# Kernel tuning notes

Measured on AMD Instinct MI355X. Metric: run time of the kernel, lower is better.

Reference implementation:

```python
import jax, jax.numpy as jnp
import numpy as np

N_NODES = 100_000
N_EDGES = 3_200_000
EPS_BN = 1e-5
EPS_NORM = 1e-12


def _sage_conv(x, src, dst, ew, pw, pb, lw, lb, rw, n_nodes):
    # project=True: relu(Linear_in->in) applied to source features
    xp = jax.nn.relu(x @ pw + pb)                       # [N, in]
    msg = xp[src] * ew[:, None]                         # [E, in] gather + weight
    agg = jax.ops.segment_sum(msg, dst, num_segments=n_nodes)      # scatter-sum
    cnt = jax.ops.segment_sum(jnp.ones_like(ew), dst, num_segments=n_nodes)
    mean = agg / jnp.maximum(cnt, 1.0)[:, None]         # scatter-mean
    out = mean @ lw + lb + x @ rw                       # neighbor lin + root lin
    # normalize=True: L2 normalize rows
    nrm = jnp.sqrt(jnp.sum(out * out, axis=-1, keepdims=True))
    return out / jnp.maximum(nrm, EPS_NORM)


def setup_inputs() -> dict:
    key = jax.random.key(0)
    ks = jax.random.split(key, 20)
    d = {}
    d["h"] = jax.random.normal(ks[0], (N_NODES, 5), dtype=jnp.float32)
    d["edge_index"] = jax.random.randint(ks[1], (2, N_EDGES), 0, N_NODES, dtype=jnp.int32)
    d["edge_weight"] = jax.random.uniform(ks[2], (N_EDGES,), dtype=jnp.float32)
    # BatchNorm1d(5) params (conv2_norm in the source is unused in forward)
    d["bn_gamma"] = jnp.ones((5,), jnp.float32)
    d["bn_beta"] = jnp.zeros((5,), jnp.float32)

    def lin(k, fan_in, fan_out):
        return jax.random.normal(k, (fan_in, fan_out), jnp.float32) * (1.0 / np.sqrt(fan_in))

    # conv1: 5 -> 64 ; conv2: 64 -> 64 (fixing source bug) ; conv3: 64 -> 5
    dims = [(5, 64), (64, 64), (64, 5)]
    ki = 3
    for i, (fi, fo) in enumerate(dims, start=1):
        d[f"c{i}_pw"] = lin(ks[ki], fi, fi); ki += 1
        d[f"c{i}_pb"] = jnp.zeros((fi,), jnp.float32)
        d[f"c{i}_lw"] = lin(ks[ki], fi, fo); ki += 1
        d[f"c{i}_lb"] = jnp.zeros((fo,), jnp.float32)
        d[f"c{i}_rw"] = lin(ks[ki], fi, fo); ki += 1
    return d


def reference(h, edge_index, edge_weight, bn_gamma, bn_beta,
              c1_pw, c1_pb, c1_lw, c1_lb, c1_rw,
              c2_pw, c2_pb, c2_lw, c2_lb, c2_rw,
              c3_pw, c3_pb, c3_lw, c3_lb, c3_rw):
    src, dst = edge_index[0], edge_index[1]
    # BatchNorm1d (training-mode batch statistics, biased variance)
    mu = jnp.mean(h, axis=0)
    var = jnp.mean((h - mu) ** 2, axis=0)
    x = (h - mu) * jax.lax.rsqrt(var + EPS_BN) * bn_gamma + bn_beta

    x = jax.nn.relu(_sage_conv(x, src, dst, edge_weight, c1_pw, c1_pb, c1_lw, c1_lb, c1_rw, N_NODES))
    x = jax.nn.relu(_sage_conv(x, src, dst, edge_weight, c2_pw, c2_pb, c2_lw, c2_lb, c2_rw, N_NODES))
    x = _sage_conv(x, src, dst, edge_weight, c3_pw, c3_pb, c3_lw, c3_lb, c3_rw, N_NODES)
    # dropout omitted (deterministic / eval-mode reference)
    return x
```

## Files before the change

kernel.cpp:

```cpp
#include <hip/hip_runtime.h>
#include <hip/hip_bf16.h>

#define N_NODES 100000
#define N_EDGES 3200000
#define BSH 8
#define NB 391

typedef __hip_bfloat16 bf16;

#define RL(v, k) __int_as_float(__builtin_amdgcn_readlane(__float_as_int(v), (k)))

__device__ __forceinline__ float loadF(const void* p, long long i, int isf32) {
    if (isf32) return ((const float*)p)[i];
    unsigned short v = ((const unsigned short*)p)[i];
    union { unsigned u; float f; } c;
    c.u = ((unsigned)v) << 16;
    return c.f;
}

__device__ __forceinline__ unsigned packEdge(int s, float w) {
    bf16 b = __float2bfloat16(w);
    unsigned short bits = *(unsigned short*)&b;
    return ((unsigned)s << 15) | (unsigned)(bits & 0x7FFF);
}
__device__ __forceinline__ int edgeSrc(unsigned u) { return (int)(u >> 15); }
__device__ __forceinline__ float edgeW(unsigned u) {
    union { unsigned x; float f; } c;
    c.x = (u & 0x7FFFu) << 16;
    return c.f;
}

#define W_GAMMA 0
#define W_BETA 8
#define W_C1PW 16
#define W_C1PB 48
#define W_C1LW 56
#define W_C1LB 376
#define W_C1RW 440
#define W_C2PW 760
#define W_C2PB 4856
#define W_C2LW 4920
#define W_C2LB 9016
#define W_C2RW 9080
#define W_C3PW 13176
#define W_C3PB 17272
#define W_C3LW 17336
#define W_C3LB 17656
#define W_C3RW 17664

__global__ void detect_dtype(const void* ew, int* flag) {
    const unsigned short* u = (const unsigned short*)ew;
    int lane = threadIdx.x;
    int big = 0;
    for (int i = lane; i < 1024; i += 64) {
        unsigned short v = u[2 * i];
        int ex = (v >> 7) & 0xFF;
        if (ex >= 128) big++;
    }
#pragma unroll
    for (int o = 32; o; o >>= 1) big += __shfl_xor(big, o, 64);
    if (lane == 0) *flag = (big > 100) ? 1 : 0;
}

__global__ void cvt_weights(const int* flag,
                            const void* p0, const void* p1, const void* p2, const void* p3,
                            const void* p4, const void* p5, const void* p6, const void* p7,
                            const void* p8, const void* p9, const void* p10, const void* p11,
                            const void* p12, const void* p13, const void* p14, const void* p15,
                            const void* p16, float* __restrict__ wts) {
    const void* ptrs[17] = {p0, p1, p2, p3, p4, p5, p6, p7, p8,
                            p9, p10, p11, p12, p13, p14, p15, p16};
    const int sz[17] = {5, 5, 25, 5, 320, 64, 320, 4096, 64,
                        4096, 64, 4096, 4096, 64, 320, 5, 320};
    const int off[17] = {W_GAMMA, W_BETA, W_C1PW, W_C1PB, W_C1LW, W_C1LB, W_C1RW,
                         W_C2PW, W_C2PB, W_C2LW, W_C2LB, W_C2RW,
                         W_C3PW, W_C3PB, W_C3LW, W_C3LB, W_C3RW};
    int t = blockIdx.x;
    int isf32 = *flag;
    for (int i = threadIdx.x; i < sz[t]; i += blockDim.x)
        wts[off[t] + i] = loadF(ptrs[t], i, isf32);
}

__global__ void bn_stats(const void* __restrict__ h, const int* __restrict__ flag,
                         float* __restrict__ stats) {
    int isf32 = *flag;
    float s[5] = {0, 0, 0, 0, 0}, q[5] = {0, 0, 0, 0, 0};
    int tid = blockIdx.x * blockDim.x + threadIdx.x;
    int stride = gridDim.x * blockDim.x;
    for (int i = tid; i < N_NODES; i += stride) {
#pragma unroll
        for (int f = 0; f < 5; f++) {
            float v = loadF(h, i * 5 + f, isf32);
            s[f] += v;
            q[f] += v * v;
        }
    }
#pragma unroll
    for (int f = 0; f < 5; f++) {
#pragma unroll
        for (int o = 32; o; o >>= 1) {
            s[f] += __shfl_xor(s[f], o, 64);
            q[f] += __shfl_xor(q[f], o, 64);
        }
    }
    __shared__ float ls[4][10];
    int wave = threadIdx.x >> 6, lane = threadIdx.x & 63;
    if (lane == 0) {
#pragma unroll
        for (int f = 0; f < 5; f++) { ls[wave][f] = s[f]; ls[wave][5 + f] = q[f]; }
    }
    __syncthreads();
    if (threadIdx.x < 10) {
        float v = ls[0][threadIdx.x] + ls[1][threadIdx.x] + ls[2][threadIdx.x] + ls[3][threadIdx.x];
        int idx = (threadIdx.x < 5) ? threadIdx.x : (threadIdx.x - 5 + 8);
        atomicAdd(&stats[idx], v);
    }
}

__global__ void bn_proj1(const void* __restrict__ h, const int* __restrict__ flag,
                         const float* __restrict__ stats, const float* __restrict__ wts,
                         float* __restrict__ xbn, float* __restrict__ xp1) {
    __shared__ float s_sc[5], s_sb[5];
    if (threadIdx.x < 5) {
        int f = threadIdx.x;
        float mean = stats[f] / (float)N_NODES;
        float var = stats[8 + f] / (float)N_NODES - mean * mean;
        float sc = wts[W_GAMMA + f] * rsqrtf(var + 1e-5f);
        s_sc[f] = sc;
        s_sb[f] = wts[W_BETA + f] - mean * sc;
    }
    __syncthreads();
    int isf32 = *flag;
    int i = blockIdx.x * blockDim.x + threadIdx.x;
    if (i >= N_NODES) return;
    float x[5];
#pragma unroll
    for (int f = 0; f < 5; f++)
        x[f] = loadF(h, i * 5 + f, isf32) * s_sc[f] + s_sb[f];
#pragma unroll
    for (int f = 0; f < 5; f++) xbn[i * 5 + f] = x[f];
#pragma unroll
    for (int j = 0; j < 5; j++) {
        float a = wts[W_C1PB + j];
#pragma unroll
        for (int k = 0; k < 5; k++) a += x[k] * wts[W_C1PW + k * 5 + j];
        xp1[i * 5 + j] = fmaxf(a, 0.f);
    }
}

__global__ void __launch_bounds__(256) bucket_hist(const int* __restrict__ dst,
                                                   int* __restrict__ bucketCnt) {
    __shared__ int hcnt[NB];
    for (int i = threadIdx.x; i < NB; i += 256) hcnt[i] = 0;
    __syncthreads();
    int per = (N_EDGES + gridDim.x - 1) / gridDim.x;
    int s = blockIdx.x * per;
    int e = min(s + per, N_EDGES);
    for (int i = s + threadIdx.x; i < e; i += 256)
        atomicAdd(&hcnt[dst[i] >> BSH], 1);
    __syncthreads();
    for (int i = threadIdx.x; i < NB; i += 256)
        if (hcnt[i]) atomicAdd(&bucketCnt[i], hcnt[i]);
}

__global__ void __launch_bounds__(512) bucket_scan(const int* __restrict__ bucketCnt,
                                                   int* __restrict__ bucketStart,
                                                   int* __restrict__ bucketCursor) {
    int tid = threadIdx.x, lane = tid & 63, w = tid >> 6;
    int v = (tid < NB) ? bucketCnt[tid] : 0;
    int sc = v;
#pragma unroll
    for (int o = 1; o < 64; o <<= 1) {
        int t = __shfl_up(sc, o, 64);
        if (lane >= o) sc += t;
    }
    __shared__ int ws[8];
    if (lane == 63) ws[w] = sc;
    __syncthreads();
    if (w == 0) {
        int wv = (lane < 8) ? ws[lane] : 0;
        int s2 = wv;
#pragma unroll
        for (int o = 1; o < 8; o <<= 1) {
            int t = __shfl_up(s2, o, 64);
            if (lane >= o) s2 += t;
        }
        if (lane < 8) ws[lane] = s2;
    }
    __syncthreads();
    int woff = w ? ws[w - 1] : 0;
    int ex = woff + sc - v;
    if (tid < NB) {
        bucketStart[tid] = ex;
        bucketCursor[tid] = ex;
    }
    if (tid == 0) bucketStart[NB] = N_EDGES;
}

__global__ void __launch_bounds__(256) bucket_stage(const int* __restrict__ src,
                                                    const int* __restrict__ dst,
                                                    const void* __restrict__ ew,
                                                    const int* __restrict__ flag,
                                                    int* __restrict__ bucketCursor,
                                                    uint2* __restrict__ stage) {
    __shared__ int hcnt[NB], cur[NB];
    int isf32 = *flag;
    for (int i = threadIdx.x; i < NB; i += 256) hcnt[i] = 0;
    __syncthreads();
    int per = (N_EDGES + gridDim.x - 1) / gridDim.x;
    int s = blockIdx.x * per;
    int e = min(s + per, N_EDGES);
    for (int i = s + threadIdx.x; i < e; i += 256)
        atomicAdd(&hcnt[dst[i] >> BSH], 1);
    __syncthreads();
    for (int i = threadIdx.x; i < NB; i += 256)
        cur[i] = hcnt[i] ? atomicAdd(&bucketCursor[i], hcnt[i]) : 0;
    __syncthreads();
    for (int i = s + threadIdx.x; i < e; i += 256) {
        int d = dst[i];
        int slot = atomicAdd(&cur[d >> BSH], 1);
        stage[slot] = make_uint2((unsigned)d, packEdge(src[i], loadF(ew, i, isf32)));
    }
}

__global__ void __launch_bounds__(256) bucket_place(const uint2* __restrict__ stage,
                                                    const int* __restrict__ bucketStart,
                                                    int* __restrict__ start,
                                                    unsigned* __restrict__ perm) {
    int b = blockIdx.x, tid = threadIdx.x;
    int base = bucketStart[b];
    int cnt = bucketStart[b + 1] - base;
    int n0 = b << BSH;
    int nn = min(256, N_NODES - n0);
    __shared__ int lcnt[256], loff[256], ws[4];
    lcnt[tid] = 0;
    __syncthreads();
    for (int i = tid; i < cnt; i += 256)
        atomicAdd(&lcnt[stage[base + i].x & 255], 1);
    __syncthreads();
    int lane = tid & 63, w = tid >> 6;
    int v = lcnt[tid];
    int sc = v;
#pragma unroll
    for (int o = 1; o < 64; o <<= 1) {
        int t = __shfl_up(sc, o, 64);
        if (lane >= o) sc += t;
    }
    if (lane == 63) ws[w] = sc;
    __syncthreads();
    int woff = 0;
    for (int k = 0; k < w; k++) woff += ws[k];
    loff[tid] = woff + sc - v;
    __syncthreads();
    if (tid < nn) start[n0 + tid] = base + loff[tid];
    if (b == 0 && tid == 0) start[N_NODES] = N_EDGES;
    lcnt[tid] = 0;
    __syncthreads();
    for (int i = tid; i < cnt; i += 256) {
        uint2 sv = stage[base + i];
        int l = sv.x & 255;
        int p = atomicAdd(&lcnt[l], 1);
        perm[base + loff[l] + p] = sv.y;
    }
}

__global__ void __launch_bounds__(256) conv1_fused(const float* __restrict__ xp1,
                                                   const float* __restrict__ xbn,
                                                   const int* __restrict__ start,
                                                   const unsigned* __restrict__ perm,
                                                   const float* __restrict__ wts,
                                                   float* __restrict__ x1,
                                                   bf16* __restrict__ y2) {
    int lane = threadIdx.x & 63;
    int wid = __builtin_amdgcn_readfirstlane((blockIdx.x * blockDim.x + threadIdx.x) >> 6);
    int nw = (gridDim.x * blockDim.x) >> 6;
    float Wlw[5], Wrw[5];
#pragma unroll
    for (int k = 0; k < 5; k++) {
        Wlw[k] = wts[W_C1LW + k * 64 + lane];
        Wrw[k] = wts[W_C1RW + k * 64 + lane];
    }
    float lb = wts[W_C1LB + lane];
    float W1[64], W2[64];
#pragma unroll
    for (int k = 0; k < 64; k++) W1[k] = wts[W_C2PW + k * 64 + lane];
#pragma unroll
    for (int k = 0; k < 64; k++) W2[k] = wts[W_C2LW + k * 64 + lane];
    float pb = wts[W_C2PB + lane];
    for (int node = wid; node < N_NODES; node += nw) {
        int e0 = start[node], e1 = start[node + 1];
        float s0 = 0, s1 = 0, s2 = 0, s3 = 0, s4 = 0;
        for (int eb = e0; eb < e1; eb += 64) {
            int e = eb + lane;
            if (e < e1) {
                unsigned p = perm[e];
                float w = edgeW(p);
                const float* row = xp1 + (size_t)edgeSrc(p) * 5;
                s0 += row[0] * w; s1 += row[1] * w; s2 += row[2] * w;
                s3 += row[3] * w; s4 += row[4] * w;
            }
        }
#pragma unroll
        for (int o = 32; o; o >>= 1) {
            s0 += __shfl_xor(s0, o, 64);
            s1 += __shfl_xor(s1, o, 64);
            s2 += __shfl_xor(s2, o, 64);
            s3 += __shfl_xor(s3, o, 64);
            s4 += __shfl_xor(s4, o, 64);
        }
        float ic = 1.f / fmaxf((float)(e1 - e0), 1.f);
        float xb = (lane < 5) ? xbn[node * 5 + lane] : 0.f;
        float out = lb + s0 * ic * Wlw[0] + s1 * ic * Wlw[1] + s2 * ic * Wlw[2] +
                    s3 * ic * Wlw[3] + s4 * ic * Wlw[4];
#pragma unroll
        for (int k = 0; k < 5; k++) out += RL(xb, k) * Wrw[k];
        float ss = out * out;
#pragma unroll
        for (int o = 32; o; o >>= 1) ss += __shfl_xor(ss, o, 64);
        float xv = fmaxf(out / fmaxf(sqrtf(ss), 1e-12f), 0.f);
        x1[(size_t)node * 64 + lane] = xv;
        float a0 = pb, a1 = 0.f, a2 = 0.f, a3 = 0.f;
#pragma unroll
        for (int k = 0; k < 64; k += 4) {
            a0 += RL(xv, k) * W1[k];
            a1 += RL(xv, k + 1) * W1[k + 1];
            a2 += RL(xv, k + 2) * W1[k + 2];
            a3 += RL(xv, k + 3) * W1[k + 3];
        }
        float xp = fmaxf((a0 + a1) + (a2 + a3), 0.f);
        float b0 = 0.f, b1 = 0.f, b2 = 0.f, b3 = 0.f;
#pragma unroll
        for (int k = 0; k < 64; k += 4) {
            b0 += RL(xp, k) * W2[k];
            b1 += RL(xp, k + 1) * W2[k + 1];
            b2 += RL(xp, k + 2) * W2[k + 2];
            b3 += RL(xp, k + 3) * W2[k + 3];
        }
        y2[(size_t)node * 64 + lane] = __float2bfloat16((b0 + b1) + (b2 + b3));
    }
}

__global__ void __launch_bounds__(256) conv2_fused_reg(const bf16* __restrict__ y2,
                                                       const int* __restrict__ start,
                                                       const unsigned* __restrict__ perm,
                                                       const float* __restrict__ x1,
                                                       const float* __restrict__ wts,
                                                       float* __restrict__ x2) {
    int lane = threadIdx.x & 63;
    int wid = __builtin_amdgcn_readfirstlane((blockIdx.x * blockDim.x + threadIdx.x) >> 6);
    int nw = (gridDim.x * blockDim.x) >> 6;
    float W[64];
#pragma unroll
    for (int k = 0; k < 64; k++) W[k] = wts[W_C2RW + k * 64 + lane];
    float lb = wts[W_C2LB + lane];
    for (int node = wid; node < N_NODES; node += nw) {
        int e0 = start[node], e1 = start[node + 1];
        float acc = 0.f;
        int e = e0;
        for (; e + 16 <= e1; e += 16) {
            unsigned p[16];
#pragma unroll
            for (int u = 0; u < 16; u++) p[u] = perm[e + u];
            float v[16];
#pragma unroll
            for (int u = 0; u < 16; u++)
                v[u] = __bfloat162float(y2[(size_t)edgeSrc(p[u]) * 64 + lane]);
#pragma unroll
            for (int u = 0; u < 16; u++) acc += v[u] * edgeW(p[u]);
        }
        for (; e + 4 <= e1; e += 4) {
            unsigned p[4];
#pragma unroll
            for (int u = 0; u < 4; u++) p[u] = perm[e + u];
            float v[4];
#pragma unroll
            for (int u = 0; u < 4; u++)
                v[u] = __bfloat162float(y2[(size_t)edgeSrc(p[u]) * 64 + lane]);
#pragma unroll
            for (int u = 0; u < 4; u++) acc += v[u] * edgeW(p[u]);
        }
        for (; e < e1; e++) {
            unsigned p = perm[e];
            acc += __bfloat162float(y2[(size_t)edgeSrc(p) * 64 + lane]) * edgeW(p);
        }
        float ic = 1.f / fmaxf((float)(e1 - e0), 1.f);
        float xv = x1[(size_t)node * 64 + lane];
        float o0 = acc * ic + lb, o1 = 0.f, o2 = 0.f, o3 = 0.f;
#pragma unroll
        for (int k = 0; k < 64; k += 4) {
            o0 += RL(xv, k) * W[k];
            o1 += RL(xv, k + 1) * W[k + 1];
            o2 += RL(xv, k + 2) * W[k + 2];
            o3 += RL(xv, k + 3) * W[k + 3];
        }
        float out = (o0 + o1) + (o2 + o3);
        float ss = out * out;
#pragma unroll
        for (int o = 32; o; o >>= 1) ss += __shfl_xor(ss, o, 64);
        float v = out / fmaxf(sqrtf(ss), 1e-12f);
        x2[(size_t)node * 64 + lane] = fmaxf(v, 0.f);
    }
}

__global__ void __launch_bounds__(256) proj3_reg(const float* __restrict__ x2,
                                                 const float* __restrict__ wts,
                                                 float* __restrict__ y3) {
    int lane = threadIdx.x & 63;
    int wid = __builtin_amdgcn_readfirstlane((blockIdx.x * blockDim.x + threadIdx.x) >> 6);
    int nw = (gridDim.x * blockDim.x) >> 6;
    float W1[64], Wl[5];
#pragma unroll
    for (int k = 0; k < 64; k++) W1[k] = wts[W_C3PW + k * 64 + lane];
#pragma unroll
    for (int j = 0; j < 5; j++) Wl[j] = wts[W_C3LW + lane * 5 + j];
    float pb = wts[W_C3PB + lane];
    for (int node = wid; node < N_NODES; node += nw) {
        float xv = x2[(size_t)node * 64 + lane];
        float a0 = pb, a1 = 0.f, a2 = 0.f, a3 = 0.f;
#pragma unroll
        for (int k = 0; k < 64; k += 4) {
            a0 += RL(xv, k) * W1[k];
            a1 += RL(xv, k + 1) * W1[k + 1];
            a2 += RL(xv, k + 2) * W1[k + 2];
            a3 += RL(xv, k + 3) * W1[k + 3];
        }
        float xp = fmaxf((a0 + a1) + (a2 + a3), 0.f);
#pragma unroll
        for (int j = 0; j < 5; j++) {
            float p = xp * Wl[j];
#pragma unroll
            for (int o = 32; o; o >>= 1) p += __shfl_xor(p, o, 64);
            if (lane == j) y3[node * 5 + j] = p;
        }
    }
}

__global__ void __launch_bounds__(256) conv3_fused(const float* __restrict__ y3,
                                                   const float* __restrict__ x2,
                                                   const int* __restrict__ start,
                                                   const unsigned* __restrict__ perm,
                                                   const float* __restrict__ wts,
                                                   const int* __restrict__ flag,
                                                   void* __restrict__ outp) {
    int lane = threadIdx.x & 63;
    int wid = __builtin_amdgcn_readfirstlane((blockIdx.x * blockDim.x + threadIdx.x) >> 6);
    int nw = (gridDim.x * blockDim.x) >> 6;
    float Wr[5];
#pragma unroll
    for (int j = 0; j < 5; j++) Wr[j] = wts[W_C3RW + lane * 5 + j];
    float lb3[5];
#pragma unroll
    for (int j = 0; j < 5; j++) lb3[j] = wts[W_C3LB + j];
    int isf32 = *flag;
    for (int node = wid; node < N_NODES; node += nw) {
        int e0 = start[node], e1 = start[node + 1];
        float s0 = 0, s1 = 0, s2 = 0, s3 = 0, s4 = 0;
        for (int eb = e0; eb < e1; eb += 64) {
            int e = eb + lane;
            if (e < e1) {
                unsigned p = perm[e];
                float w = edgeW(p);
                const float* row = y3 + (size_t)edgeSrc(p) * 5;
                s0 += row[0] * w; s1 += row[1] * w; s2 += row[2] * w;
                s3 += row[3] * w; s4 += row[4] * w;
            }
        }
#pragma unroll
        for (int o = 32; o; o >>= 1) {
            s0 += __shfl_xor(s0, o, 64);
            s1 += __shfl_xor(s1, o, 64);
            s2 += __shfl_xor(s2, o, 64);
            s3 += __shfl_xor(s3, o, 64);
            s4 += __shfl_xor(s4, o, 64);
        }
        float ic = 1.f / fmaxf((float)(e1 - e0), 1.f);
        float xv = x2[(size_t)node * 64 + lane];
        float m[5] = {s0 * ic, s1 * ic, s2 * ic, s3 * ic, s4 * ic};
        float r[5], ss = 0.f;
#pragma unroll
        for (int j = 0; j < 5; j++) {
            float p = xv * Wr[j];
#pragma unroll
            for (int o = 32; o; o >>= 1) p += __shfl_xor(p, o, 64);
            r[j] = p + m[j] + lb3[j];
            ss += r[j] * r[j];
        }
        float inv = 1.f / fmaxf(sqrtf(ss), 1e-12f);
#pragma unroll
        for (int j = 0; j < 5; j++) {
            if (lane == j) {
                float v = r[j] * inv;
                if (isf32) ((float*)outp)[node * 5 + j] = v;
                else ((bf16*)outp)[node * 5 + j] = __float2bfloat16(v);
            }
        }
    }
}

extern "C" void kernel_launch(void* const* d_in, const int* in_sizes, int n_in,
                              void* d_out, int out_size, void* d_ws, size_t ws_size,
                              hipStream_t stream) {
    const void* h = d_in[0];
    const int* ei = (const int*)d_in[1];
    const int* src = ei;
    const int* dst = ei + N_EDGES;
    const void* ew = d_in[2];

    float* W = (float*)d_ws;
    int* flag = (int*)W;
    float* stats = W + 16;
    float* wts = W + 64;
    float* xbn = W + 20480;
    float* xp1 = xbn + N_NODES * 5;
    int* startp = (int*)(xp1 + N_NODES * 5);
    int* bucketCnt = startp + N_NODES + 64;
    int* bucketStart = bucketCnt + NB + 1;
    int* bucketCursor = bucketStart + NB + 1;
    unsigned* perm = (unsigned*)(bucketCursor + NB + 62);
    float* x1 = (float*)(perm + N_EDGES);
    uint2* stage = (uint2*)x1;
    bf16* y2 = (bf16*)(x1 + (size_t)N_NODES * 64);
    float* x2 = x1;
    float* y3 = xp1;

    detect_dtype<<<1, 64, 0, stream>>>(ew, flag);
    cvt_weights<<<17, 256, 0, stream>>>(flag,
        d_in[3], d_in[4],
        d_in[5], d_in[6], d_in[7], d_in[8], d_in[9],
        d_in[10], d_in[11], d_in[12], d_in[13], d_in[14],
        d_in[15], d_in[16], d_in[17], d_in[18], d_in[19],
        wts);

    hipMemsetAsync(stats, 0, 32 * sizeof(float), stream);
    hipMemsetAsync(bucketCnt, 0, NB * sizeof(int), stream);

    bn_stats<<<200, 256, 0, stream>>>(h, flag, stats);
    bn_proj1<<<(N_NODES + 255) / 256, 256, 0, stream>>>(h, flag, stats, wts, xbn, xp1);

    bucket_hist<<<256, 256, 0, stream>>>(dst, bucketCnt);
    bucket_scan<<<1, 512, 0, stream>>>(bucketCnt, bucketStart, bucketCursor);
    bucket_stage<<<256, 256, 0, stream>>>(src, dst, ew, flag, bucketCursor, stage);
    bucket_place<<<NB, 256, 0, stream>>>(stage, bucketStart, startp, perm);

    conv1_fused<<<2048, 256, 0, stream>>>(xp1, xbn, startp, perm, wts, x1, y2);

    conv2_fused_reg<<<4096, 256, 0, stream>>>(y2, startp, perm, x1, wts, x2);

    proj3_reg<<<1024, 256, 0, stream>>>(x2, wts, y3);
    conv3_fused<<<2048, 256, 0, stream>>>(y3, x2, startp, perm, wts, flag, d_out);
}
```

Measured before the change: 574.1 us.

## Fuse layer-3 projection into conv2 and pad 5-wide node rows to 8 floats

The layer-3 projection (relu(x2·W3p + b) followed by the 5-wide neighbor linear) is folded into the conv2 kernel's epilogue, so x2 no longer has to be re-read by a separate kernel and one launch is dropped. The 5-float per-node rows for xp1 and y3 are padded to a stride of 8 so that the conv1 and conv3 edge gathers can use one aligned float4 load plus one scalar load. The bucket histogram and staging kernels also get twice as many blocks. The cost is 69 more weight registers held per lane in conv2, which may lower occupancy for its latency-bound gather, and the padded rows take more workspace memory.

```diff
diff --git a/kernel.cpp b/kernel.cpp
--- a/kernel.cpp
+++ b/kernel.cpp
@@ -144,7 +144,7 @@
         float a = wts[W_C1PB + j];
 #pragma unroll
         for (int k = 0; k < 5; k++) a += x[k] * wts[W_C1PW + k * 5 + j];
-        xp1[i * 5 + j] = fmaxf(a, 0.f);
+        xp1[i * 8 + j] = fmaxf(a, 0.f);
     }
 }
 
@@ -295,9 +295,11 @@
             if (e < e1) {
                 unsigned p = perm[e];
                 float w = edgeW(p);
-                const float* row = xp1 + (size_t)edgeSrc(p) * 5;
-                s0 += row[0] * w; s1 += row[1] * w; s2 += row[2] * w;
-                s3 += row[3] * w; s4 += row[4] * w;
+                const float* row = xp1 + (size_t)edgeSrc(p) * 8;
+                float4 v4 = *(const float4*)row;
+                float v5 = row[4];
+                s0 += v4.x * w; s1 += v4.y * w; s2 += v4.z * w;
+                s3 += v4.w * w; s4 += v5 * w;
             }
         }
 #pragma unroll
@@ -340,12 +342,13 @@
     }
 }
 
-__global__ void __launch_bounds__(256) conv2_fused_reg(const bf16* __restrict__ y2,
-                                                       const int* __restrict__ start,
-                                                       const unsigned* __restrict__ perm,
-                                                       const float* __restrict__ x1,
-                                                       const float* __restrict__ wts,
-                                                       float* __restrict__ x2) {
+__global__ void __launch_bounds__(256) conv2_fused3(const bf16* __restrict__ y2,
+                                                    const int* __restrict__ start,
+                                                    const unsigned* __restrict__ perm,
+                                                    const float* __restrict__ x1,
+                                                    const float* __restrict__ wts,
+                                                    float* __restrict__ x2,
+                                                    float* __restrict__ y3) {
     int lane = threadIdx.x & 63;
     int wid = __builtin_amdgcn_readfirstlane((blockIdx.x * blockDim.x + threadIdx.x) >> 6);
     int nw = (gridDim.x * blockDim.x) >> 6;
@@ -353,6 +356,12 @@
 #pragma unroll
     for (int k = 0; k < 64; k++) W[k] = wts[W_C2RW + k * 64 + lane];
     float lb = wts[W_C2LB + lane];
+    float W3[64], Wl3[5];
+#pragma unroll
+    for (int k = 0; k < 64; k++) W3[k] = wts[W_C3PW + k * 64 + lane];
+#pragma unroll
+    for (int j = 0; j < 5; j++) Wl3[j] = wts[W_C3LW + lane * 5 + j];
+    float pb3 = wts[W_C3PB + lane];
     for (int node = wid; node < N_NODES; node += nw) {
         int e0 = start[node], e1 = start[node + 1];
         float acc = 0.f;
@@ -397,40 +406,23 @@
         float ss = out * out;
 #pragma unroll
         for (int o = 32; o; o >>= 1) ss += __shfl_xor(ss, o, 64);
-        float v = out / fmaxf(sqrtf(ss), 1e-12f);
-        x2[(size_t)node * 64 + lane] = fmaxf(v, 0.f);
-    }
-}
-
-__global__ void __launch_bounds__(256) proj3_reg(const float* __restrict__ x2,
-                                                 const float* __restrict__ wts,
-                                                 float* __restrict__ y3) {
-    int lane = threadIdx.x & 63;
-    int wid = __builtin_amdgcn_readfirstlane((blockIdx.x * blockDim.x + threadIdx.x) >> 6);
-    int nw = (gridDim.x * blockDim.x) >> 6;
-    float W1[64], Wl[5];
-#pragma unroll
-    for (int k = 0; k < 64; k++) W1[k] = wts[W_C3PW + k * 64 + lane];
-#pragma unroll
-    for (int j = 0; j < 5; j++) Wl[j] = wts[W_C3LW + lane * 5 + j];
-    float pb = wts[W_C3PB + lane];
-    for (int node = wid; node < N_NODES; node += nw) {
-        float xv = x2[(size_t)node * 64 + lane];
-        float a0 = pb, a1 = 0.f, a2 = 0.f, a3 = 0.f;
+        float x2v = fmaxf(out / fmaxf(sqrtf(ss), 1e-12f), 0.f);
+        x2[(size_t)node * 64 + lane] = x2v;
+        float a0 = pb3, a1 = 0.f, a2 = 0.f, a3 = 0.f;
 #pragma unroll
         for (int k = 0; k < 64; k += 4) {
-            a0 += RL(xv, k) * W1[k];
-            a1 += RL(xv, k + 1) * W1[k + 1];
-            a2 += RL(xv, k + 2) * W1[k + 2];
-            a3 += RL(xv, k + 3) * W1[k + 3];
+            a0 += RL(x2v, k) * W3[k];
+            a1 += RL(x2v, k + 1) * W3[k + 1];
+            a2 += RL(x2v, k + 2) * W3[k + 2];
+            a3 += RL(x2v, k + 3) * W3[k + 3];
         }
         float xp = fmaxf((a0 + a1) + (a2 + a3), 0.f);
 #pragma unroll
         for (int j = 0; j < 5; j++) {
-            float p = xp * Wl[j];
+            float p = xp * Wl3[j];
 #pragma unroll
             for (int o = 32; o; o >>= 1) p += __shfl_xor(p, o, 64);
-            if (lane == j) y3[node * 5 + j] = p;
+            if (lane == j) y3[(size_t)node * 8 + j] = p;
         }
     }
 }
@@ -460,9 +452,11 @@
             if (e < e1) {
                 unsigned p = perm[e];
                 float w = edgeW(p);
-                const float* row = y3 + (size_t)edgeSrc(p) * 5;
-                s0 += row[0] * w; s1 += row[1] * w; s2 += row[2] * w;
-                s3 += row[3] * w; s4 += row[4] * w;
+                const float* row = y3 + (size_t)edgeSrc(p) * 8;
+                float4 v4 = *(const float4*)row;
+                float v5 = row[4];
+                s0 += v4.x * w; s1 += v4.y * w; s2 += v4.z * w;
+                s3 += v4.w * w; s4 += v5 * w;
             }
         }
 #pragma unroll
@@ -512,7 +506,7 @@
     float* wts = W + 64;
     float* xbn = W + 20480;
     float* xp1 = xbn + N_NODES * 5;
-    int* startp = (int*)(xp1 + N_NODES * 5);
+    int* startp = (int*)(xp1 + N_NODES * 8);
     int* bucketCnt = startp + N_NODES + 64;
     int* bucketStart = bucketCnt + NB + 1;
     int* bucketCursor = bucketStart + NB + 1;
@@ -537,15 +531,14 @@
     bn_stats<<<200, 256, 0, stream>>>(h, flag, stats);
     bn_proj1<<<(N_NODES + 255) / 256, 256, 0, stream>>>(h, flag, stats, wts, xbn, xp1);
 
-    bucket_hist<<<256, 256, 0, stream>>>(dst, bucketCnt);
+    bucket_hist<<<512, 256, 0, stream>>>(dst, bucketCnt);
     bucket_scan<<<1, 512, 0, stream>>>(bucketCnt, bucketStart, bucketCursor);
-    bucket_stage<<<256, 256, 0, stream>>>(src, dst, ew, flag, bucketCursor, stage);
+    bucket_stage<<<512, 256, 0, stream>>>(src, dst, ew, flag, bucketCursor, stage);
     bucket_place<<<NB, 256, 0, stream>>>(stage, bucketStart, startp, perm);
 
     conv1_fused<<<2048, 256, 0, stream>>>(xp1, xbn, startp, perm, wts, x1, y2);
 
-    conv2_fused_reg<<<4096, 256, 0, stream>>>(y2, startp, perm, x1, wts, x2);
-
-    proj3_reg<<<1024, 256, 0, stream>>>(x2, wts, y3);
+    conv2_fused3<<<4096, 256, 0, stream>>>(y2, startp, perm, x1, wts, x2, y3);
+
     conv3_fused<<<2048, 256, 0, stream>>>(y3, x2, startp, perm, wts, flag, d_out);
 }
```

Measured after the change: 597.2 us. +4.0%, slower.
